# Optimization experiments

Hardware: AMD Instinct MI355X
Metric: run time of the kernel (lower is better)

Reference implementation:

```python
import jax, jax.numpy as jnp
import numpy as np

DIM = 128   # EMBED_DIM
NH = 4      # N_HEADS
HD = DIM // NH          # 32
NT = max(1, int(NH * 0.25))  # 1 timelike head
NS = NH - NT                 # 3 spacelike heads
TD = NT * HD                 # T_DIM = 32
SD = 6      # STATE_DIM
TIN, TOUT = 20, 20
NL = 3      # N_LAYERS
B, T = 4096, TIN + TOUT      # seq len capped by pos embedding (40)


def _ln(x, g, b):
    m = jnp.mean(x, -1, keepdims=True)
    v = jnp.mean((x - m) ** 2, -1, keepdims=True)
    return g * (x - m) * jax.lax.rsqrt(v + 1e-5) + b


def _mln(x, pg, pb, g, b):
    # MinkowskiLN: standard LN then scale by |sum(s^2)-sum(t^2)| norm
    x = _ln(x, pg, pb)
    t = x[..., :TD]
    s = x[..., TD:]
    mq = jnp.sum(s * s, -1, keepdims=True) - jnp.sum(t * t, -1, keepdims=True)
    eps = jnp.maximum(0.01 * jnp.mean(jnp.abs(mq)), 1e-5)
    return g * (x / (jnp.sqrt(jnp.abs(mq) + eps) + eps)) + b


def _attn(h, qt, kt, qs, ks, vw, ow, ob, ws):
    # Minkowski attention (mode='f3'): timelike scores negated with learned sigmoid weight
    Bb, Tt, _ = h.shape
    scale = HD ** -0.5
    Qt = (h @ qt).reshape(Bb, Tt, NT, HD)
    Kt = (h @ kt).reshape(Bb, Tt, NT, HD)
    Qs = (h @ qs).reshape(Bb, Tt, NS, HD)
    Ks = (h @ ks).reshape(Bb, Tt, NS, HD)
    st = jnp.einsum('bthd,bshd->bths', Qt, Kt)  # [B,T,NT,T]
    ss = jnp.einsum('bthd,bshd->bths', Qs, Ks)  # [B,T,NS,T]
    score = jnp.concatenate([-jax.nn.sigmoid(ws) * st, ss], axis=2) * scale
    a = jax.nn.softmax(score, axis=-1)
    V = (h @ vw).reshape(Bb, Tt, NH, HD)
    o = jnp.einsum('bths,bshd->bthd', a, V).reshape(Bb, Tt, DIM)
    return o @ ow + ob


def setup_inputs() -> dict:
    key = jax.random.key(0)
    ks = iter(jax.random.split(key, 32))
    def w(shape, s=0.02):
        return (jax.random.normal(next(ks), shape, jnp.float32) * s).astype(jnp.float32)
    inp = {
        'x': jax.random.normal(next(ks), (B, T, SD), jnp.float32),
        'embed_w': w((SD, DIM)), 'embed_b': jnp.zeros((DIM,), jnp.float32),
        'pos': w((TIN + TOUT, DIM)),
        'qt_w': w((NL, DIM, NT * HD)), 'kt_w': w((NL, DIM, NT * HD)),
        'qs_w': w((NL, DIM, NS * HD)), 'ks_w': w((NL, DIM, NS * HD)),
        'v_w': w((NL, DIM, DIM)), 'out_w': w((NL, DIM, DIM)), 'out_b': jnp.zeros((NL, DIM), jnp.float32),
        'w_sigma': jnp.zeros((NL,), jnp.float32),
        'n1_pre_g': jnp.ones((NL, DIM), jnp.float32), 'n1_pre_b': jnp.zeros((NL, DIM), jnp.float32),
        'n1_g': jnp.ones((NL, DIM), jnp.float32), 'n1_b': jnp.zeros((NL, DIM), jnp.float32),
        'n2_pre_g': jnp.ones((NL, DIM), jnp.float32), 'n2_pre_b': jnp.zeros((NL, DIM), jnp.float32),
        'n2_g': jnp.ones((NL, DIM), jnp.float32), 'n2_b': jnp.zeros((NL, DIM), jnp.float32),
        'ff_w1': w((NL, DIM, 4 * DIM)), 'ff_b1': jnp.zeros((NL, 4 * DIM), jnp.float32),
        'ff_w2': w((NL, 4 * DIM, DIM)), 'ff_b2': jnp.zeros((NL, DIM), jnp.float32),
        'fn_pre_g': jnp.ones((DIM,), jnp.float32), 'fn_pre_b': jnp.zeros((DIM,), jnp.float32),
        'fn_g': jnp.ones((DIM,), jnp.float32), 'fn_b': jnp.zeros((DIM,), jnp.float32),
        'traj_w': w((DIM, SD * TOUT)), 'traj_b': jnp.zeros((SD * TOUT,), jnp.float32),
    }
    return inp


def reference(x, embed_w, embed_b, pos, qt_w, kt_w, qs_w, ks_w, v_w, out_w, out_b,
              w_sigma, n1_pre_g, n1_pre_b, n1_g, n1_b, n2_pre_g, n2_pre_b, n2_g, n2_b,
              ff_w1, ff_b1, ff_w2, ff_b2, fn_pre_g, fn_pre_b, fn_g, fn_b, traj_w, traj_b):
    Tt = x.shape[1]
    h = x @ embed_w + embed_b + pos[:Tt]  # [B,T,D]
    for i in range(NL):
        h = h + _attn(_mln(h, n1_pre_g[i], n1_pre_b[i], n1_g[i], n1_b[i]),
                      qt_w[i], kt_w[i], qs_w[i], ks_w[i], v_w[i], out_w[i], out_b[i], w_sigma[i])
        hn = _mln(h, n2_pre_g[i], n2_pre_b[i], n2_g[i], n2_b[i])
        h = h + (jax.nn.gelu(hn @ ff_w1[i] + ff_b1[i], approximate=False) @ ff_w2[i] + ff_b2[i])
    h = _mln(h, fn_pre_g, fn_pre_b, fn_g, fn_b)[:, -1, :]  # [B,D]
    out = h @ traj_w + traj_b
    return out.reshape(x.shape[0], TOUT, SD)
```

## Files before the change

### kernel.cpp

```cpp
#include <hip/hip_runtime.h>
#include <hip/hip_bf16.h>

#define DIMM 128
#define TT   40
#define BB   4096
#define NTOK (BB*TT)
#define NLAY 3

typedef float f4 __attribute__((ext_vector_type(4)));
typedef float f32x4 __attribute__((ext_vector_type(4)));
typedef short bf16x8 __attribute__((ext_vector_type(8)));

__device__ __forceinline__ float bf2f(unsigned short u) {
    union { unsigned int i; float f; } v; v.i = ((unsigned int)u) << 16; return v.f;
}
__device__ __forceinline__ unsigned short f2bu(float f) {
    __hip_bfloat16 h = __float2bfloat16(f);
    return *reinterpret_cast<unsigned short*>(&h);
}
__device__ __forceinline__ float gelu_f(float v) {
    float z = 1.5957691216057308f * fmaf(0.044715f * v * v, v, v);
    return v / (1.f + __expf(-z));
}

__device__ __forceinline__ void mln_rowstat(
    const float* v, const float* pgv, const float* pbv,
    float& m, float& rstd, float& mq)
{
    float s1 = 0.f, s2 = 0.f;
    #pragma unroll
    for (int nf = 0; nf < 8; ++nf) { s1 += v[nf]; s2 += v[nf]*v[nf]; }
    #pragma unroll
    for (int o = 1; o < 16; o <<= 1) { s1 += __shfl_xor(s1, o); s2 += __shfl_xor(s2, o); }
    m = s1 * (1.f/128.f);
    float var = s2 * (1.f/128.f) - m*m;
    rstd = rsqrtf(fmaxf(var, 0.f) + 1e-5f);
    float q = 0.f;
    #pragma unroll
    for (int nf = 0; nf < 8; ++nf) {
        float yv = (v[nf] - m) * rstd * pgv[nf] + pbv[nf];
        q += (nf < 2 ? -(yv*yv) : (yv*yv));
    }
    #pragma unroll
    for (int o = 1; o < 16; o <<= 1) q += __shfl_xor(q, o);
    mq = q;
}

__device__ __forceinline__ void build_mln_frags(
    bf16x8 a[2][4], const float* __restrict__ h, int row_mf0, int row_mf1,
    const float* __restrict__ stats, float eps,
    const float* __restrict__ pg, const float* __restrict__ pb,
    const float* __restrict__ gg, const float* __restrict__ gb, int q)
{
    int rows[2] = { row_mf0, row_mf1 };
    float rss3[2], mm[2], s3v[2];
    #pragma unroll
    for (int mf = 0; mf < 2; ++mf) {
        int r = rows[mf];
        float m  = stats[(size_t)r*4 + 0];
        float rs = stats[(size_t)r*4 + 1];
        float mq = stats[(size_t)r*4 + 2];
        float s3 = 1.f / (sqrtf(fabsf(mq) + eps) + eps);
        rss3[mf] = rs * s3; mm[mf] = -m * rss3[mf]; s3v[mf] = s3;
    }
    #pragma unroll
    for (int ks = 0; ks < 4; ++ks) {
        int c0 = ks*32 + q*8;
        float al[8], be[8], gbv[8];
        #pragma unroll
        for (int j = 0; j < 8; ++j) {
            float g = gg[c0+j];
            al[j] = g * pg[c0+j]; be[j] = g * pb[c0+j]; gbv[j] = gb[c0+j];
        }
        #pragma unroll
        for (int mf = 0; mf < 2; ++mf) {
            int r = rows[mf];
            f4 x0 = *(const f4*)(h + (size_t)r*128 + c0);
            f4 x1 = *(const f4*)(h + (size_t)r*128 + c0 + 4);
            union { unsigned short u[8]; bf16x8 v; } o;
            #pragma unroll
            for (int j = 0; j < 4; ++j) {
                float t0 = fmaf(x0[j], rss3[mf], mm[mf]);
                float t1 = fmaf(x1[j], rss3[mf], mm[mf]);
                o.u[j]   = f2bu(fmaf(al[j],   t0, fmaf(be[j],   s3v[mf], gbv[j])));
                o.u[j+4] = f2bu(fmaf(al[j+4], t1, fmaf(be[j+4], s3v[mf], gbv[j+4])));
            }
            a[mf][ks] = o.v;
        }
    }
}

__global__ __launch_bounds__(256) void pack_w_k(
    const float* __restrict__ qt, const float* __restrict__ kt,
    const float* __restrict__ qs, const float* __restrict__ ks,
    const float* __restrict__ vw, const float* __restrict__ ow,
    const float* __restrict__ w1, const float* __restrict__ w2,
    unsigned short* __restrict__ wqT, unsigned short* __restrict__ outT,
    unsigned short* __restrict__ ff1T, unsigned short* __restrict__ ff2T)
{
    int idx = blockIdx.x * 256 + threadIdx.x;
    if (idx < 147456) {
        int i = idx / 49152, r = idx % 49152;
        int n = r / 128, k = r % 128;
        float v;
        if (n < 32)        v = qt[i*4096  + k*32  + n];
        else if (n < 64)   v = kt[i*4096  + k*32  + (n-32)];
        else if (n < 160)  v = qs[i*12288 + k*96  + (n-64)];
        else if (n < 256)  v = ks[i*12288 + k*96  + (n-160)];
        else               v = vw[i*16384 + k*128 + (n-256)];
        wqT[idx] = f2bu(v);
    } else if (idx < 196608) {
        int j = idx - 147456;
        int i = j / 16384, r = j % 16384;
        int n = r / 128, k = r % 128;
        outT[j] = f2bu(ow[i*16384 + k*128 + n]);
    } else if (idx < 393216) {
        int j = idx - 196608;
        int i = j / 65536, r = j % 65536;
        int n = r / 128, k = r % 128;
        ff1T[j] = f2bu(w1[i*65536 + k*512 + n]);
    } else {
        int j = idx - 393216;
        int i = j / 65536, r = j % 65536;
        int n = r / 512, k = r % 512;
        ff2T[j] = f2bu(w2[i*65536 + k*128 + n]);
    }
}

__global__ __launch_bounds__(256) void embed_k(
    const float* __restrict__ x, const float* __restrict__ ew,
    const float* __restrict__ eb, const float* __restrict__ pos,
    float* __restrict__ h)
{
    int idx = blockIdx.x * 256 + threadIdx.x;
    int n = idx >> 7, d = idx & 127;
    int t = n % TT;
    const float* xr = x + (size_t)n * 6;
    float acc = eb[d] + pos[t*128 + d];
    #pragma unroll
    for (int k = 0; k < 6; ++k) acc += xr[k] * ew[k*128 + d];
    h[idx] = acc;
}

__global__ __launch_bounds__(256) void mln_stats_k(
    const float* __restrict__ h, const float* __restrict__ pg, const float* __restrict__ pb,
    float* __restrict__ stats, float* __restrict__ partials)
{
    int wid = threadIdx.x >> 6, lane = threadIdx.x & 63;
    int tok = blockIdx.x * 4 + wid;
    const float* hr = h + (size_t)tok * 128;
    float x0 = hr[lane], x1 = hr[lane + 64];
    float s = x0 + x1;
    #pragma unroll
    for (int o = 32; o > 0; o >>= 1) s += __shfl_xor(s, o);
    float m = s * (1.f / 128.f);
    float d0 = x0 - m, d1 = x1 - m;
    float v = d0*d0 + d1*d1;
    #pragma unroll
    for (int o = 32; o > 0; o >>= 1) v += __shfl_xor(v, o);
    float rstd = rsqrtf(v * (1.f / 128.f) + 1e-5f);
    float y0 = d0 * rstd * pg[lane]      + pb[lane];
    float y1 = d1 * rstd * pg[lane + 64] + pb[lane + 64];
    float q = (lane < 32 ? -(y0*y0) : (y0*y0)) + y1*y1;
    #pragma unroll
    for (int o = 32; o > 0; o >>= 1) q += __shfl_xor(q, o);
    if (lane == 0) {
        stats[(size_t)tok*4 + 0] = m;
        stats[(size_t)tok*4 + 1] = rstd;
        stats[(size_t)tok*4 + 2] = q;
    }
    __shared__ float pm[4];
    if (lane == 0) pm[wid] = fabsf(q);
    __syncthreads();
    if (threadIdx.x == 0) partials[blockIdx.x] = (pm[0] + pm[1]) + (pm[2] + pm[3]);
}

__global__ __launch_bounds__(1024) void reduce_eps_k(
    const float* __restrict__ partials, int n, float* __restrict__ scal)
{
    float s = 0.f;
    for (int i = threadIdx.x; i < n; i += 1024) s += partials[i];
    __shared__ float sm[1024];
    sm[threadIdx.x] = s;
    __syncthreads();
    for (int o = 512; o > 0; o >>= 1) {
        if (threadIdx.x < o) sm[threadIdx.x] += sm[threadIdx.x + o];
        __syncthreads();
    }
    if (threadIdx.x == 0) {
        float mean = sm[0] / (float)NTOK;
        scal[0] = fmaxf(0.01f * mean, 1e-5f);
    }
}

__global__ __launch_bounds__(256) void qkv_k(
    const float* __restrict__ hsrc,
    const float* __restrict__ stats_in, const float* __restrict__ scal,
    const float* __restrict__ pg, const float* __restrict__ pb,
    const float* __restrict__ gg, const float* __restrict__ gb,
    const unsigned short* __restrict__ BT,
    unsigned short* __restrict__ obuf)
{
    __shared__ unsigned char Wl[32768];
    const int tid = threadIdx.x, wid = tid >> 6, lane = tid & 63;
    const int q = lane >> 4, l15 = lane & 15;
    const int row0 = blockIdx.x * 128;
    const int wrow = row0 + wid * 32;

    bf16x8 a[2][4];
    build_mln_frags(a, hsrc, wrow + l15, wrow + 16 + l15,
                    stats_in, scal[0], pg, pb, gg, gb, q);

    const unsigned char* BTb = (const unsigned char*)BT;
    for (int nc = 0; nc < 3; ++nc) {
        __syncthreads();
        {
            int row = tid >> 1, half = tid & 1;
            #pragma unroll
            for (int jj = 0; jj < 8; ++jj) {
                int colb = half*128 + jj*16;
                uint4 v = *(const uint4*)(BTb + (size_t)(nc*128 + row)*256 + colb);
                *(uint4*)(Wl + row*256 + (colb ^ ((row & 7) << 4))) = v;
            }
        }
        __syncthreads();
        f32x4 acc[2][8] = {};
        #pragma unroll
        for (int ks = 0; ks < 4; ++ks)
            #pragma unroll
            for (int nf = 0; nf < 8; ++nf) {
                int row = nf*16 + l15;
                bf16x8 b = *(const bf16x8*)(Wl + row*256 + ((ks*64 + q*16) ^ ((row & 7) << 4)));
                #pragma unroll
                for (int mf = 0; mf < 2; ++mf)
                    acc[mf][nf] = __builtin_amdgcn_mfma_f32_16x16x32_bf16(a[mf][ks], b, acc[mf][nf], 0, 0, 0);
            }
        #pragma unroll
        for (int mf = 0; mf < 2; ++mf)
            #pragma unroll
            for (int r = 0; r < 4; ++r) {
                int row = wrow + mf*16 + q*4 + r;
                #pragma unroll
                for (int nf = 0; nf < 8; ++nf)
                    obuf[(size_t)row*384 + nc*128 + nf*16 + l15] = f2bu(acc[mf][nf][r]);
            }
    }
}

__global__ __launch_bounds__(256) void attn_k(
    const unsigned short* __restrict__ scratch, const float* __restrict__ wsp,
    const unsigned short* __restrict__ outT,
    const float* __restrict__ bias,
    float* __restrict__ hres,
    const float* __restrict__ pre_g, const float* __restrict__ pre_b,
    float* __restrict__ stats, float* __restrict__ partials)
{
    __shared__ unsigned char lds[45056];
    __shared__ float sm[16];
    const int b = blockIdx.x, tid = threadIdx.x;
    const unsigned short* base = scratch + (size_t)b * TT * 384;

    unsigned char* VtL = lds;
    unsigned char* PlL = lds + 16384;

    for (int e = tid; e < 1536; e += 256) {
        int hh = e / 384, rem = e - hh*384;
        int row = rem >> 3, c = rem & 7;
        int byte = hh*6144 + ((row*128 + 96 + 4*c) ^ ((row & 7) << 4));
        *(unsigned int*)(PlL + byte) = 0u;
    }
    for (int e = tid; e < 1536; e += 256) {
        int hh = e / 384, rem = e - hh*384;
        int d = rem / 12, sc2 = rem - d*12;
        int s = 40 + 2*sc2;
        int byte = hh*4096 + ((d*128 + s*2) ^ (((d >> 3) & 7) << 4));
        *(unsigned int*)(VtL + byte) = 0u;
    }
    for (int e = tid; e < 640; e += 256) {
        int s = e >> 4, ck = e & 15;
        union { bf16x8 v; unsigned short u[8]; } g;
        g.v = *(const bf16x8*)(base + (size_t)s*384 + 256 + ck*8);
        int hh = ck >> 2, d0 = (ck & 3) * 8;
        #pragma unroll
        for (int j = 0; j < 8; ++j) {
            int d = d0 + j;
            int byte = hh*4096 + ((d*128 + s*2) ^ (((d >> 3) & 7) << 4));
            *(unsigned short*)(VtL + byte) = g.u[j];
        }
    }
    __syncthreads();

    const int h = tid >> 6, lane = tid & 63;
    const int l15 = lane & 15, q4 = lane >> 4;
    const unsigned char* Vt = VtL + h*4096;
    unsigned char* Pl = PlL + h*6144;

    const int qcol = (h == 0) ? 0  : 32  + h*32;
    const int kcol = (h == 0) ? 32 : 128 + h*32;
    const float scale = 0.17677669529663687f;
    const float wmul = (h == 0) ? (-scale / (1.f + __expf(-wsp[0]))) : scale;

    bf16x8 aq[3], bk[3];
    #pragma unroll
    for (int mt = 0; mt < 3; ++mt) {
        int t = l15 + 16*mt; if (t > 39) t = 39;
        aq[mt] = *(const bf16x8*)(base + (size_t)t*384 + qcol + q4*8);
    }
    #pragma unroll
    for (int jt = 0; jt < 3; ++jt) {
        int s = l15 + 16*jt; if (s > 39) s = 39;
        bk[jt] = *(const bf16x8*)(base + (size_t)s*384 + kcol + q4*8);
    }
    f32x4 sc[3][3] = {};
    #pragma unroll
    for (int mt = 0; mt < 3; ++mt)
        #pragma unroll
        for (int jt = 0; jt < 3; ++jt)
            sc[mt][jt] = __builtin_amdgcn_mfma_f32_16x16x32_bf16(aq[mt], bk[jt], sc[mt][jt], 0, 0, 0);

    const bool mask2 = (l15 >= 8);
    float inv[3][4];
    #pragma unroll
    for (int mt = 0; mt < 3; ++mt) {
        #pragma unroll
        for (int r = 0; r < 4; ++r) {
            float s0 = wmul * sc[mt][0][r];
            float s1 = wmul * sc[mt][1][r];
            float s2 = mask2 ? -1e30f : wmul * sc[mt][2][r];
            float mx = fmaxf(fmaxf(s0, s1), s2);
            #pragma unroll
            for (int o = 1; o < 16; o <<= 1) mx = fmaxf(mx, __shfl_xor(mx, o));
            float e0 = __expf(s0 - mx), e1 = __expf(s1 - mx), e2 = __expf(s2 - mx);
            float sum = e0 + e1 + e2;
            #pragma unroll
            for (int o = 1; o < 16; o <<= 1) sum += __shfl_xor(sum, o);
            inv[mt][r] = 1.f / sum;
            int row = 16*mt + 4*q4 + r;
            int rsw = (row & 7) << 4;
            *(unsigned short*)(Pl + ((row*128 + l15*2       ) ^ rsw)) = f2bu(e0);
            *(unsigned short*)(Pl + ((row*128 + 32 + l15*2  ) ^ rsw)) = f2bu(e1);
            *(unsigned short*)(Pl + ((row*128 + 64 + l15*2  ) ^ rsw)) = f2bu(e2);
        }
    }

    f32x4 oacc[3][2] = {};
    #pragma unroll
    for (int ks2 = 0; ks2 < 2; ++ks2) {
        bf16x8 bv[2];
        #pragma unroll
        for (int nt = 0; nt < 2; ++nt) {
            int d = l15 + 16*nt;
            bv[nt] = *(const bf16x8*)(Vt + ((d*128 + 64*ks2 + 16*q4) ^ (((d >> 3) & 7) << 4)));
        }
        #pragma unroll
        for (int mt = 0; mt < 3; ++mt) {
            int row = l15 + 16*mt;
            bf16x8 pa = *(const bf16x8*)(Pl + ((row*128 + 64*ks2 + 16*q4) ^ ((row & 7) << 4)));
            #pragma unroll
            for (int nt = 0; nt < 2; ++nt)
                oacc[mt][nt] = __builtin_amdgcn_mfma_f32_16x16x32_bf16(pa, bv[nt], oacc[mt][nt], 0, 0, 0);
        }
    }

    __syncthreads();
    unsigned char* Ol = lds;
    unsigned char* Wl = lds + 12288;

    #pragma unroll
    for (int mt = 0; mt < 3; ++mt) {
        #pragma unroll
        for (int r = 0; r < 4; ++r) {
            int row = 16*mt + 4*q4 + r;
            float iv = inv[mt][r];
            int rsw = (row & 7) << 4;
            #pragma unroll
            for (int nt = 0; nt < 2; ++nt) {
                int colb = (h*32 + nt*16 + l15) * 2;
                *(unsigned short*)(Ol + ((row*256 + colb) ^ rsw)) = f2bu(oacc[mt][nt][r] * iv);
            }
        }
    }
    {
        const unsigned char* BTb = (const unsigned char*)outT;
        int row = tid >> 1, half = tid & 1;
        #pragma unroll
        for (int jj = 0; jj < 8; ++jj) {
            int colb = half*128 + jj*16;
            uint4 v = *(const uint4*)(BTb + (size_t)row*256 + colb);
            *(uint4*)(Wl + row*256 + (colb ^ ((row & 7) << 4))) = v;
        }
    }
    if (h == 3 && l15 == 0) sm[12 + q4] = 0.f;
    __syncthreads();

    if (h < 3) {
        int arow = 16*h + l15;
        bf16x8 ao[4];
        #pragma unroll
        for (int ks = 0; ks < 4; ++ks)
            ao[ks] = *(const bf16x8*)(Ol + arow*256 + ((ks*64 + q4*16) ^ ((arow & 7) << 4)));
        f32x4 oc[8] = {};
        #pragma unroll
        for (int ks = 0; ks < 4; ++ks)
            #pragma unroll
            for (int nf = 0; nf < 8; ++nf) {
                int brow = nf*16 + l15;
                bf16x8 bo = *(const bf16x8*)(Wl + brow*256 + ((ks*64 + q4*16) ^ ((brow & 7) << 4)));
                oc[nf] = __builtin_amdgcn_mfma_f32_16x16x32_bf16(ao[ks], bo, oc[nf], 0, 0, 0);
            }

        float bv[8], pgv[8], pbv[8];
        #pragma unroll
        for (int nf = 0; nf < 8; ++nf) {
            int c = nf*16 + l15;
            bv[nf] = bias[c]; pgv[nf] = pre_g[c]; pbv[nf] = pre_b[c];
        }
        float amq = 0.f;
        #pragma unroll
        for (int r = 0; r < 4; ++r) {
            int t = 16*h + 4*q4 + r;
            if (t < 40) {
                int row = b*TT + t;
                float* hr = hres + (size_t)row*128;
                float v[8];
                #pragma unroll
                for (int nf = 0; nf < 8; ++nf) {
                    float hv = hr[nf*16 + l15] + oc[nf][r] + bv[nf];
                    hr[nf*16 + l15] = hv;
                    v[nf] = hv;
                }
                float m, rstd, mq;
                mln_rowstat(v, pgv, pbv, m, rstd, mq);
                if (l15 == 0) {
                    stats[(size_t)row*4 + 0] = m;
                    stats[(size_t)row*4 + 1] = rstd;
                    stats[(size_t)row*4 + 2] = mq;
                }
                amq += fabsf(mq);
            }
        }
        if (l15 == 0) sm[h*4 + q4] = amq;
    }
    __syncthreads();
    if (tid == 0) {
        float s = 0.f;
        #pragma unroll
        for (int j = 0; j < 16; ++j) s += sm[j];
        partials[b] = s;
    }
}

__global__ __launch_bounds__(256) void ffn_k(
    const float* __restrict__ hsrc,
    const float* __restrict__ stats_in, const float* __restrict__ scal,
    const float* __restrict__ m2_pre_g, const float* __restrict__ m2_pre_b,
    const float* __restrict__ m2_g, const float* __restrict__ m2_b,
    const unsigned short* __restrict__ W1T,
    const float* __restrict__ b1,
    const unsigned short* __restrict__ W2T,
    const float* __restrict__ b2,
    float* __restrict__ h,
    const float* __restrict__ pre_g, const float* __restrict__ pre_b,
    float* __restrict__ stats, float* __restrict__ partials)
{
    __shared__ unsigned char W1l[16384];
    __shared__ unsigned char W2l[16384];
    __shared__ unsigned char Ps[4][32*144];
    __shared__ float sm[16];
    const int tid = threadIdx.x, wid = tid >> 6, lane = tid & 63;
    const int q = lane >> 4, l15 = lane & 15;
    const int row0 = blockIdx.x * 128;
    const int wrow = row0 + wid * 32;
    unsigned char* Pw = Ps[wid];

    bf16x8 a[2][4];
    build_mln_frags(a, hsrc, wrow + l15, wrow + 16 + l15,
                    stats_in, scal[0], m2_pre_g, m2_pre_b, m2_g, m2_b, q);

    float b2v[8];
    #pragma unroll
    for (int nf = 0; nf < 8; ++nf) b2v[nf] = b2[nf*16 + l15];

    f32x4 acc2[2][8] = {};
    const unsigned char* W1b = (const unsigned char*)W1T;
    const unsigned char* W2b = (const unsigned char*)W2T;

    for (int c = 0; c < 8; ++c) {
        __syncthreads();
        {
            int row = tid >> 2, seg = tid & 3;
            #pragma unroll
            for (int jj = 0; jj < 4; ++jj) {
                int colb = seg*64 + jj*16;
                uint4 v = *(const uint4*)(W1b + (size_t)(c*64 + row)*256 + colb);
                *(uint4*)(W1l + row*256 + (colb ^ ((row & 7) << 4))) = v;
            }
        }
        {
            int row = tid >> 1, seg = tid & 1;
            #pragma unroll
            for (int jj = 0; jj < 4; ++jj) {
                int colb = seg*64 + jj*16;
                uint4 v = *(const uint4*)(W2b + (size_t)row*1024 + c*128 + colb);
                *(uint4*)(W2l + row*128 + (colb ^ ((row & 7) << 4))) = v;
            }
        }
        __syncthreads();
        float bbv[4];
        #pragma unroll
        for (int nf = 0; nf < 4; ++nf) bbv[nf] = b1[c*64 + nf*16 + l15];
        f32x4 acc1[2][4];
        #pragma unroll
        for (int mf = 0; mf < 2; ++mf)
            #pragma unroll
            for (int nf = 0; nf < 4; ++nf)
                acc1[mf][nf] = f32x4{bbv[nf], bbv[nf], bbv[nf], bbv[nf]};
        #pragma unroll
        for (int ks = 0; ks < 4; ++ks)
            #pragma unroll
            for (int nf = 0; nf < 4; ++nf) {
                int row = nf*16 + l15;
                bf16x8 b = *(const bf16x8*)(W1l + row*256 + ((ks*64 + q*16) ^ ((row & 7) << 4)));
                #pragma unroll
                for (int mf = 0; mf < 2; ++mf)
                    acc1[mf][nf] = __builtin_amdgcn_mfma_f32_16x16x32_bf16(a[mf][ks], b, acc1[mf][nf], 0, 0, 0);
            }
        #pragma unroll
        for (int nf = 0; nf < 4; ++nf) {
            #pragma unroll
            for (int mf = 0; mf < 2; ++mf) {
                #pragma unroll
                for (int r = 0; r < 4; ++r) {
                    float v = gelu_f(acc1[mf][nf][r]);
                    *(unsigned short*)(Pw + (mf*16 + q*4 + r)*144 + (nf*16 + l15)*2) = f2bu(v);
                }
            }
        }
        #pragma unroll
        for (int ks2 = 0; ks2 < 2; ++ks2) {
            bf16x8 a2[2];
            #pragma unroll
            for (int mf = 0; mf < 2; ++mf)
                a2[mf] = *(const bf16x8*)(Pw + (mf*16 + l15)*144 + ks2*64 + q*16);
            #pragma unroll
            for (int nf = 0; nf < 8; ++nf) {
                int row = nf*16 + l15;
                bf16x8 b = *(const bf16x8*)(W2l + row*128 + ((ks2*64 + q*16) ^ ((row & 7) << 4)));
                #pragma unroll
                for (int mf = 0; mf < 2; ++mf)
                    acc2[mf][nf] = __builtin_amdgcn_mfma_f32_16x16x32_bf16(a2[mf], b, acc2[mf][nf], 0, 0, 0);
            }
        }
    }

    float pgv[8], pbv[8];
    #pragma unroll
    for (int nf = 0; nf < 8; ++nf) { pgv[nf] = pre_g[nf*16 + l15]; pbv[nf] = pre_b[nf*16 + l15]; }
    float amq = 0.f;
    #pragma unroll
    for (int mf = 0; mf < 2; ++mf) {
        #pragma unroll
        for (int r = 0; r < 4; ++r) {
            int row = wrow + mf*16 + q*4 + r;
            float* hr = h + (size_t)row*128;
            float v[8];
            #pragma unroll
            for (int nf = 0; nf < 8; ++nf) {
                float hv = hr[nf*16 + l15] + acc2[mf][nf][r] + b2v[nf];
                hr[nf*16 + l15] = hv;
                v[nf] = hv;
            }
            float m, rstd, mq;
            mln_rowstat(v, pgv, pbv, m, rstd, mq);
            if (l15 == 0) {
                stats[(size_t)row*4 + 0] = m;
                stats[(size_t)row*4 + 1] = rstd;
                stats[(size_t)row*4 + 2] = mq;
            }
            amq += fabsf(mq);
        }
    }
    if (l15 == 0) sm[wid*4 + q] = amq;
    __syncthreads();
    if (tid == 0) {
        float s = 0.f;
        #pragma unroll
        for (int j = 0; j < 16; ++j) s += sm[j];
        partials[blockIdx.x] = s;
    }
}

__global__ __launch_bounds__(128) void head_k(
    const float* __restrict__ h, const float* __restrict__ stats, const float* __restrict__ scal,
    const float* __restrict__ pg, const float* __restrict__ pb,
    const float* __restrict__ gg, const float* __restrict__ gb,
    const float* __restrict__ tw, const float* __restrict__ tb,
    float* __restrict__ out)
{
    int b = blockIdx.x, tid = threadIdx.x;
    int tok = b*TT + (TT - 1);
    __shared__ float ys[128];
    float eps = scal[0];
    float m  = stats[(size_t)tok*4 + 0];
    float rs = stats[(size_t)tok*4 + 1];
    float mq = stats[(size_t)tok*4 + 2];
    float s3 = 1.f / (sqrtf(fabsf(mq) + eps) + eps);
    float x = h[(size_t)tok*128 + tid];
    ys[tid] = gg[tid] * (((x - m) * rs * pg[tid] + pb[tid]) * s3) + gb[tid];
    __syncthreads();
    if (tid < 120) {
        float acc = tb[tid];
        #pragma unroll 4
        for (int d = 0; d < 128; ++d) acc += ys[d] * tw[d*120 + tid];
        out[(size_t)b*120 + tid] = acc;
    }
}

extern "C" void kernel_launch(void* const* d_in, const int* in_sizes, int n_in,
                              void* d_out, int out_size, void* d_ws, size_t ws_size,
                              hipStream_t stream) {
    const float* x        = (const float*)d_in[0];
    const float* embed_w  = (const float*)d_in[1];
    const float* embed_b  = (const float*)d_in[2];
    const float* pos      = (const float*)d_in[3];
    const float* qt_w     = (const float*)d_in[4];
    const float* kt_w     = (const float*)d_in[5];
    const float* qs_w     = (const float*)d_in[6];
    const float* ks_w     = (const float*)d_in[7];
    const float* v_w      = (const float*)d_in[8];
    const float* out_w    = (const float*)d_in[9];
    const float* out_b    = (const float*)d_in[10];
    const float* w_sigma  = (const float*)d_in[11];
    const float* n1_pre_g = (const float*)d_in[12];
    const float* n1_pre_b = (const float*)d_in[13];
    const float* n1_g     = (const float*)d_in[14];
    const float* n1_b     = (const float*)d_in[15];
    const float* n2_pre_g = (const float*)d_in[16];
    const float* n2_pre_b = (const float*)d_in[17];
    const float* n2_g     = (const float*)d_in[18];
    const float* n2_b     = (const float*)d_in[19];
    const float* ff_w1    = (const float*)d_in[20];
    const float* ff_b1    = (const float*)d_in[21];
    const float* ff_w2    = (const float*)d_in[22];
    const float* ff_b2    = (const float*)d_in[23];
    const float* fn_pre_g = (const float*)d_in[24];
    const float* fn_pre_b = (const float*)d_in[25];
    const float* fn_g     = (const float*)d_in[26];
    const float* fn_b     = (const float*)d_in[27];
    const float* traj_w   = (const float*)d_in[28];
    const float* traj_b   = (const float*)d_in[29];

    char* ws = (char*)d_ws;
    float*          h        = (float*)ws;
    float*          stats    = (float*)(ws + 83886080);
    unsigned short* scratch  = (unsigned short*)(ws + 86507520);
    unsigned short* wqT      = (unsigned short*)(ws + 212336640);
    unsigned short* outT     = (unsigned short*)(ws + 212631552);
    unsigned short* ff1T     = (unsigned short*)(ws + 212729856);
    unsigned short* ff2T     = (unsigned short*)(ws + 213123072);
    float*          partials = (float*)(ws + 213516288);
    float*          scal     = (float*)(ws + 213680128);

    pack_w_k<<<2304, 256, 0, stream>>>(qt_w, kt_w, qs_w, ks_w, v_w, out_w, ff_w1, ff_w2,
                                       wqT, outT, ff1T, ff2T);
    embed_k<<<81920, 256, 0, stream>>>(x, embed_w, embed_b, pos, h);

    mln_stats_k<<<40960, 256, 0, stream>>>(h, n1_pre_g, n1_pre_b, stats, partials);
    reduce_eps_k<<<1, 1024, 0, stream>>>(partials, 40960, scal);

    for (int i = 0; i < NLAY; ++i) {
        qkv_k<<<1280, 256, 0, stream>>>(
            h, stats, scal,
            n1_pre_g + i*128, n1_pre_b + i*128, n1_g + i*128, n1_b + i*128,
            wqT + (size_t)i*49152, scratch);
        attn_k<<<4096, 256, 0, stream>>>(
            scratch, w_sigma + i,
            outT + (size_t)i*16384, out_b + i*128,
            h, n2_pre_g + i*128, n2_pre_b + i*128,
            stats, partials);
        reduce_eps_k<<<1, 1024, 0, stream>>>(partials, 4096, scal);
        const float* npg = (i < NLAY-1) ? (n1_pre_g + (i+1)*128) : fn_pre_g;
        const float* npb = (i < NLAY-1) ? (n1_pre_b + (i+1)*128) : fn_pre_b;
        ffn_k<<<1280, 256, 0, stream>>>(
            h, stats, scal,
            n2_pre_g + i*128, n2_pre_b + i*128, n2_g + i*128, n2_b + i*128,
            ff1T + (size_t)i*65536, ff_b1 + i*512,
            ff2T + (size_t)i*65536, ff_b2 + i*128, h,
            npg, npb, stats, partials);
        reduce_eps_k<<<1, 1024, 0, stream>>>(partials, 1280, scal);
    }

    head_k<<<4096, 128, 0, stream>>>(h, stats, scal, fn_pre_g, fn_pre_b, fn_g, fn_b,
                                     traj_w, traj_b, (float*)d_out);
}
```

Measured before the change: 909.0 us.

## Register-prefetch weight tiles to overlap global loads with compute

Weight tiles for the QKV, attention output-projection and FFN kernels are now loaded from global memory into registers ahead of time, either before the LN fragment build or during the previous chunk's MFMA loop. Each chunk then only writes registers to LDS, which is meant to hide global-load latency behind compute. The cost is extra register pressure (up to 8 uint4 held per thread), which could lower occupancy or cause spills.

```diff
diff --git a/kernel.cpp b/kernel.cpp
--- a/kernel.cpp
+++ b/kernel.cpp
@@ -207,21 +207,28 @@
     const int row0 = blockIdx.x * 128;
     const int wrow = row0 + wid * 32;
 
+    const unsigned char* BTb = (const unsigned char*)BT;
+    const int srow = tid >> 1, shalf = tid & 1;
+    uint4 wr[8];
+    #pragma unroll
+    for (int jj = 0; jj < 8; ++jj)
+        wr[jj] = *(const uint4*)(BTb + (size_t)srow*256 + shalf*128 + jj*16);
+
     bf16x8 a[2][4];
     build_mln_frags(a, hsrc, wrow + l15, wrow + 16 + l15,
                     stats_in, scal[0], pg, pb, gg, gb, q);
 
-    const unsigned char* BTb = (const unsigned char*)BT;
     for (int nc = 0; nc < 3; ++nc) {
         __syncthreads();
-        {
-            int row = tid >> 1, half = tid & 1;
-            #pragma unroll
-            for (int jj = 0; jj < 8; ++jj) {
-                int colb = half*128 + jj*16;
-                uint4 v = *(const uint4*)(BTb + (size_t)(nc*128 + row)*256 + colb);
-                *(uint4*)(Wl + row*256 + (colb ^ ((row & 7) << 4))) = v;
-            }
+        #pragma unroll
+        for (int jj = 0; jj < 8; ++jj) {
+            int colb = shalf*128 + jj*16;
+            *(uint4*)(Wl + srow*256 + (colb ^ ((srow & 7) << 4))) = wr[jj];
+        }
+        if (nc < 2) {
+            #pragma unroll
+            for (int jj = 0; jj < 8; ++jj)
+                wr[jj] = *(const uint4*)(BTb + (size_t)((nc+1)*128 + srow)*256 + shalf*128 + jj*16);
         }
         __syncthreads();
         f32x4 acc[2][8] = {};
@@ -260,6 +267,15 @@
     const int b = blockIdx.x, tid = threadIdx.x;
     const unsigned short* base = scratch + (size_t)b * TT * 384;
 
+    const int srow = tid >> 1, shalf = tid & 1;
+    uint4 wout_r[8];
+    {
+        const unsigned char* BTb = (const unsigned char*)outT;
+        #pragma unroll
+        for (int jj = 0; jj < 8; ++jj)
+            wout_r[jj] = *(const uint4*)(BTb + (size_t)srow*256 + shalf*128 + jj*16);
+    }
+
     unsigned char* VtL = lds;
     unsigned char* PlL = lds + 16384;
 
@@ -380,15 +396,10 @@
             }
         }
     }
-    {
-        const unsigned char* BTb = (const unsigned char*)outT;
-        int row = tid >> 1, half = tid & 1;
-        #pragma unroll
-        for (int jj = 0; jj < 8; ++jj) {
-            int colb = half*128 + jj*16;
-            uint4 v = *(const uint4*)(BTb + (size_t)row*256 + colb);
-            *(uint4*)(Wl + row*256 + (colb ^ ((row & 7) << 4))) = v;
-        }
+    #pragma unroll
+    for (int jj = 0; jj < 8; ++jj) {
+        int colb = shalf*128 + jj*16;
+        *(uint4*)(Wl + srow*256 + (colb ^ ((srow & 7) << 4))) = wout_r[jj];
     }
     if (h == 3 && l15 == 0) sm[12 + q4] = 0.f;
     __syncthreads();
@@ -473,6 +484,18 @@
     const int wrow = row0 + wid * 32;
     unsigned char* Pw = Ps[wid];
 
+    const unsigned char* W1b = (const unsigned char*)W1T;
+    const unsigned char* W2b = (const unsigned char*)W2T;
+    const int s1row = tid >> 2, s1seg = tid & 3;
+    const int s2row = tid >> 1, s2seg = tid & 1;
+
+    uint4 w1r[4], w2r[4];
+    #pragma unroll
+    for (int jj = 0; jj < 4; ++jj) {
+        w1r[jj] = *(const uint4*)(W1b + (size_t)s1row*256 + s1seg*64 + jj*16);
+        w2r[jj] = *(const uint4*)(W2b + (size_t)s2row*1024 + s2seg*64 + jj*16);
+    }
+
     bf16x8 a[2][4];
     build_mln_frags(a, hsrc, wrow + l15, wrow + 16 + l15,
                     stats_in, scal[0], m2_pre_g, m2_pre_b, m2_g, m2_b, q);
@@ -482,27 +505,21 @@
     for (int nf = 0; nf < 8; ++nf) b2v[nf] = b2[nf*16 + l15];
 
     f32x4 acc2[2][8] = {};
-    const unsigned char* W1b = (const unsigned char*)W1T;
-    const unsigned char* W2b = (const unsigned char*)W2T;
 
     for (int c = 0; c < 8; ++c) {
         __syncthreads();
-        {
-            int row = tid >> 2, seg = tid & 3;
+        #pragma unroll
+        for (int jj = 0; jj < 4; ++jj) {
+            int colb1 = s1seg*64 + jj*16;
+            *(uint4*)(W1l + s1row*256 + (colb1 ^ ((s1row & 7) << 4))) = w1r[jj];
+            int colb2 = s2seg*64 + jj*16;
+            *(uint4*)(W2l + s2row*128 + (colb2 ^ ((s2row & 7) << 4))) = w2r[jj];
+        }
+        if (c < 7) {
             #pragma unroll
             for (int jj = 0; jj < 4; ++jj) {
-                int colb = seg*64 + jj*16;
-                uint4 v = *(const uint4*)(W1b + (size_t)(c*64 + row)*256 + colb);
-                *(uint4*)(W1l + row*256 + (colb ^ ((row & 7) << 4))) = v;
-            }
-        }
-        {
-            int row = tid >> 1, seg = tid & 1;
-            #pragma unroll
-            for (int jj = 0; jj < 4; ++jj) {
-                int colb = seg*64 + jj*16;
-                uint4 v = *(const uint4*)(W2b + (size_t)row*1024 + c*128 + colb);
-                *(uint4*)(W2l + row*128 + (colb ^ ((row & 7) << 4))) = v;
+                w1r[jj] = *(const uint4*)(W1b + (size_t)((c+1)*64 + s1row)*256 + s1seg*64 + jj*16);
+                w2r[jj] = *(const uint4*)(W2b + (size_t)s2row*1024 + (c+1)*128 + s2seg*64 + jj*16);
             }
         }
         __syncthreads();
```

Measured after the change: 1.490 ms. 1.64x slower.

## Fuse QKV projection into attention kernel, keep Q/K/V in LDS

Applied to the files above, without the earlier changes.

Merges the MinkowskiLN-normalized QKV projection into the per-sequence attention kernel. Each block computes Q, K and V for its 40 tokens with MFMA, stores Q/K in swizzled LDS and V transposed in LDS, and skips the global bf16 scratch round trip. This removes one kernel launch and the write and read of a large scratch buffer. In exchange, weight fragments are read from global or cache by every block without LDS staging, and 48 rows are padded per 40-token sequence, which wastes some MFMA work.

```diff
diff --git a/kernel.cpp b/kernel.cpp
--- a/kernel.cpp
+++ b/kernel.cpp
@@ -193,62 +193,13 @@
     }
 }
 
-__global__ __launch_bounds__(256) void qkv_k(
+__global__ __launch_bounds__(256) void fattn_k(
     const float* __restrict__ hsrc,
     const float* __restrict__ stats_in, const float* __restrict__ scal,
     const float* __restrict__ pg, const float* __restrict__ pb,
     const float* __restrict__ gg, const float* __restrict__ gb,
-    const unsigned short* __restrict__ BT,
-    unsigned short* __restrict__ obuf)
-{
-    __shared__ unsigned char Wl[32768];
-    const int tid = threadIdx.x, wid = tid >> 6, lane = tid & 63;
-    const int q = lane >> 4, l15 = lane & 15;
-    const int row0 = blockIdx.x * 128;
-    const int wrow = row0 + wid * 32;
-
-    bf16x8 a[2][4];
-    build_mln_frags(a, hsrc, wrow + l15, wrow + 16 + l15,
-                    stats_in, scal[0], pg, pb, gg, gb, q);
-
-    const unsigned char* BTb = (const unsigned char*)BT;
-    for (int nc = 0; nc < 3; ++nc) {
-        __syncthreads();
-        {
-            int row = tid >> 1, half = tid & 1;
-            #pragma unroll
-            for (int jj = 0; jj < 8; ++jj) {
-                int colb = half*128 + jj*16;
-                uint4 v = *(const uint4*)(BTb + (size_t)(nc*128 + row)*256 + colb);
-                *(uint4*)(Wl + row*256 + (colb ^ ((row & 7) << 4))) = v;
-            }
-        }
-        __syncthreads();
-        f32x4 acc[2][8] = {};
-        #pragma unroll
-        for (int ks = 0; ks < 4; ++ks)
-            #pragma unroll
-            for (int nf = 0; nf < 8; ++nf) {
-                int row = nf*16 + l15;
-                bf16x8 b = *(const bf16x8*)(Wl + row*256 + ((ks*64 + q*16) ^ ((row & 7) << 4)));
-                #pragma unroll
-                for (int mf = 0; mf < 2; ++mf)
-                    acc[mf][nf] = __builtin_amdgcn_mfma_f32_16x16x32_bf16(a[mf][ks], b, acc[mf][nf], 0, 0, 0);
-            }
-        #pragma unroll
-        for (int mf = 0; mf < 2; ++mf)
-            #pragma unroll
-            for (int r = 0; r < 4; ++r) {
-                int row = wrow + mf*16 + q*4 + r;
-                #pragma unroll
-                for (int nf = 0; nf < 8; ++nf)
-                    obuf[(size_t)row*384 + nc*128 + nf*16 + l15] = f2bu(acc[mf][nf][r]);
-            }
-    }
-}
-
-__global__ __launch_bounds__(256) void attn_k(
-    const unsigned short* __restrict__ scratch, const float* __restrict__ wsp,
+    const unsigned short* __restrict__ wqT,
+    const float* __restrict__ wsp,
     const unsigned short* __restrict__ outT,
     const float* __restrict__ bias,
     float* __restrict__ hres,
@@ -258,17 +209,12 @@
     __shared__ unsigned char lds[45056];
     __shared__ float sm[16];
     const int b = blockIdx.x, tid = threadIdx.x;
-    const unsigned short* base = scratch + (size_t)b * TT * 384;
-
-    unsigned char* VtL = lds;
-    unsigned char* PlL = lds + 16384;
-
-    for (int e = tid; e < 1536; e += 256) {
-        int hh = e / 384, rem = e - hh*384;
-        int row = rem >> 3, c = rem & 7;
-        int byte = hh*6144 + ((row*128 + 96 + 4*c) ^ ((row & 7) << 4));
-        *(unsigned int*)(PlL + byte) = 0u;
-    }
+    const int h = tid >> 6, lane = tid & 63;
+    const int l15 = lane & 15, q4 = lane >> 4;
+
+    unsigned char* QKl = lds;
+    unsigned char* VtL = lds + 24576;
+
     for (int e = tid; e < 1536; e += 256) {
         int hh = e / 384, rem = e - hh*384;
         int d = rem / 12, sc2 = rem - d*12;
@@ -276,25 +222,89 @@
         int byte = hh*4096 + ((d*128 + s*2) ^ (((d >> 3) & 7) << 4));
         *(unsigned int*)(VtL + byte) = 0u;
     }
-    for (int e = tid; e < 640; e += 256) {
-        int s = e >> 4, ck = e & 15;
-        union { bf16x8 v; unsigned short u[8]; } g;
-        g.v = *(const bf16x8*)(base + (size_t)s*384 + 256 + ck*8);
-        int hh = ck >> 2, d0 = (ck & 3) * 8;
-        #pragma unroll
-        for (int j = 0; j < 8; ++j) {
-            int d = d0 + j;
-            int byte = hh*4096 + ((d*128 + s*2) ^ (((d >> 3) & 7) << 4));
-            *(unsigned short*)(VtL + byte) = g.u[j];
-        }
-    }
-    __syncthreads();
-
-    const int h = tid >> 6, lane = tid & 63;
-    const int l15 = lane & 15, q4 = lane >> 4;
+
+    const int rowbase = b * TT;
+    int rows[3];
+    #pragma unroll
+    for (int mt = 0; mt < 3; ++mt) { int t = l15 + 16*mt; if (t > 39) t = 39; rows[mt] = rowbase + t; }
+    bf16x8 a3[3][4];
+    {
+        float eps = scal[0];
+        float rss3[3], mm3[3], s3v[3];
+        #pragma unroll
+        for (int mt = 0; mt < 3; ++mt) {
+            int r = rows[mt];
+            float m  = stats_in[(size_t)r*4 + 0];
+            float rs = stats_in[(size_t)r*4 + 1];
+            float mq = stats_in[(size_t)r*4 + 2];
+            float s3 = 1.f / (sqrtf(fabsf(mq) + eps) + eps);
+            rss3[mt] = rs * s3; mm3[mt] = -m * rss3[mt]; s3v[mt] = s3;
+        }
+        #pragma unroll
+        for (int ks = 0; ks < 4; ++ks) {
+            int c0 = ks*32 + q4*8;
+            float al[8], be[8], gbv[8];
+            #pragma unroll
+            for (int j = 0; j < 8; ++j) {
+                float g = gg[c0+j];
+                al[j] = g * pg[c0+j]; be[j] = g * pb[c0+j]; gbv[j] = gb[c0+j];
+            }
+            #pragma unroll
+            for (int mt = 0; mt < 3; ++mt) {
+                int r = rows[mt];
+                f4 x0 = *(const f4*)(hsrc + (size_t)r*128 + c0);
+                f4 x1 = *(const f4*)(hsrc + (size_t)r*128 + c0 + 4);
+                union { unsigned short u[8]; bf16x8 v; } o;
+                #pragma unroll
+                for (int j = 0; j < 4; ++j) {
+                    float t0 = fmaf(x0[j], rss3[mt], mm3[mt]);
+                    float t1 = fmaf(x1[j], rss3[mt], mm3[mt]);
+                    o.u[j]   = f2bu(fmaf(al[j],   t0, fmaf(be[j],   s3v[mt], gbv[j])));
+                    o.u[j+4] = f2bu(fmaf(al[j+4], t1, fmaf(be[j+4], s3v[mt], gbv[j+4])));
+                }
+                a3[mt][ks] = o.v;
+            }
+        }
+    }
+
+    #pragma unroll
+    for (int nt = 0; nt < 6; ++nt) {
+        int tile = h*6 + nt;
+        f32x4 acc[3] = {};
+        #pragma unroll
+        for (int ks = 0; ks < 4; ++ks) {
+            bf16x8 bfrag = *(const bf16x8*)(wqT + (size_t)(tile*16 + l15)*128 + ks*32 + q4*8);
+            #pragma unroll
+            for (int mt = 0; mt < 3; ++mt)
+                acc[mt] = __builtin_amdgcn_mfma_f32_16x16x32_bf16(a3[mt][ks], bfrag, acc[mt], 0, 0, 0);
+        }
+        if (tile < 16) {
+            #pragma unroll
+            for (int mt = 0; mt < 3; ++mt)
+                #pragma unroll
+                for (int r = 0; r < 4; ++r) {
+                    int row = 16*mt + 4*q4 + r;
+                    int colb = (tile*16 + l15)*2;
+                    *(unsigned short*)(QKl + ((row*256 + colb) ^ ((row & 7) << 4))) = f2bu(acc[mt][r]);
+                }
+        } else {
+            int dfull = tile*16 + l15 - 256;
+            int hh = dfull >> 5, d = dfull & 31;
+            #pragma unroll
+            for (int mt = 0; mt < 3; ++mt)
+                #pragma unroll
+                for (int r = 0; r < 4; ++r) {
+                    int s = 16*mt + 4*q4 + r;
+                    if (s < 40) {
+                        int byte = hh*4096 + ((d*128 + s*2) ^ (((d >> 3) & 7) << 4));
+                        *(unsigned short*)(VtL + byte) = f2bu(acc[mt][r]);
+                    }
+                }
+        }
+    }
+    __syncthreads();
+
     const unsigned char* Vt = VtL + h*4096;
-    unsigned char* Pl = PlL + h*6144;
-
     const int qcol = (h == 0) ? 0  : 32  + h*32;
     const int kcol = (h == 0) ? 32 : 128 + h*32;
     const float scale = 0.17677669529663687f;
@@ -304,19 +314,27 @@
     #pragma unroll
     for (int mt = 0; mt < 3; ++mt) {
         int t = l15 + 16*mt; if (t > 39) t = 39;
-        aq[mt] = *(const bf16x8*)(base + (size_t)t*384 + qcol + q4*8);
+        aq[mt] = *(const bf16x8*)(QKl + ((t*256 + qcol*2 + q4*16) ^ ((t & 7) << 4)));
     }
     #pragma unroll
     for (int jt = 0; jt < 3; ++jt) {
         int s = l15 + 16*jt; if (s > 39) s = 39;
-        bk[jt] = *(const bf16x8*)(base + (size_t)s*384 + kcol + q4*8);
-    }
-    f32x4 sc[3][3] = {};
+        bk[jt] = *(const bf16x8*)(QKl + ((s*256 + kcol*2 + q4*16) ^ ((s & 7) << 4)));
+    }
+    f32x4 sc9[3][3] = {};
     #pragma unroll
     for (int mt = 0; mt < 3; ++mt)
         #pragma unroll
         for (int jt = 0; jt < 3; ++jt)
-            sc[mt][jt] = __builtin_amdgcn_mfma_f32_16x16x32_bf16(aq[mt], bk[jt], sc[mt][jt], 0, 0, 0);
+            sc9[mt][jt] = __builtin_amdgcn_mfma_f32_16x16x32_bf16(aq[mt], bk[jt], sc9[mt][jt], 0, 0, 0);
+
+    __syncthreads();
+
+    unsigned char* Pl = lds + h*6144;
+    for (int e = lane; e < 384; e += 64) {
+        int row = e >> 3, c = e & 7;
+        *(unsigned int*)(Pl + ((row*128 + 96 + 4*c) ^ ((row & 7) << 4))) = 0u;
+    }
 
     const bool mask2 = (l15 >= 8);
     float inv[3][4];
@@ -324,9 +342,9 @@
     for (int mt = 0; mt < 3; ++mt) {
         #pragma unroll
         for (int r = 0; r < 4; ++r) {
-            float s0 = wmul * sc[mt][0][r];
-            float s1 = wmul * sc[mt][1][r];
-            float s2 = mask2 ? -1e30f : wmul * sc[mt][2][r];
+            float s0 = wmul * sc9[mt][0][r];
+            float s1 = wmul * sc9[mt][1][r];
+            float s2 = mask2 ? -1e30f : wmul * sc9[mt][2][r];
             float mx = fmaxf(fmaxf(s0, s1), s2);
             #pragma unroll
             for (int o = 1; o < 16; o <<= 1) mx = fmaxf(mx, __shfl_xor(mx, o));
@@ -653,13 +671,12 @@
     char* ws = (char*)d_ws;
     float*          h        = (float*)ws;
     float*          stats    = (float*)(ws + 83886080);
-    unsigned short* scratch  = (unsigned short*)(ws + 86507520);
-    unsigned short* wqT      = (unsigned short*)(ws + 212336640);
-    unsigned short* outT     = (unsigned short*)(ws + 212631552);
-    unsigned short* ff1T     = (unsigned short*)(ws + 212729856);
-    unsigned short* ff2T     = (unsigned short*)(ws + 213123072);
-    float*          partials = (float*)(ws + 213516288);
-    float*          scal     = (float*)(ws + 213680128);
+    unsigned short* wqT      = (unsigned short*)(ws + 86507520);
+    unsigned short* outT     = (unsigned short*)(ws + 86802432);
+    unsigned short* ff1T     = (unsigned short*)(ws + 86900736);
+    unsigned short* ff2T     = (unsigned short*)(ws + 87293952);
+    float*          partials = (float*)(ws + 87687168);
+    float*          scal     = (float*)(ws + 87851008);
 
     pack_w_k<<<2304, 256, 0, stream>>>(qt_w, kt_w, qs_w, ks_w, v_w, out_w, ff_w1, ff_w2,
                                        wqT, outT, ff1T, ff2T);
@@ -669,12 +686,10 @@
     reduce_eps_k<<<1, 1024, 0, stream>>>(partials, 40960, scal);
 
     for (int i = 0; i < NLAY; ++i) {
-        qkv_k<<<1280, 256, 0, stream>>>(
+        fattn_k<<<4096, 256, 0, stream>>>(
             h, stats, scal,
             n1_pre_g + i*128, n1_pre_b + i*128, n1_g + i*128, n1_b + i*128,
-            wqT + (size_t)i*49152, scratch);
-        attn_k<<<4096, 256, 0, stream>>>(
-            scratch, w_sigma + i,
+            wqT + (size_t)i*49152, w_sigma + i,
             outT + (size_t)i*16384, out_b + i*128,
             h, n2_pre_g + i*128, n2_pre_b + i*128,
             stats, partials);
```

After: 1.029 ms. 1.13x slower.
